# Kernel optimization log

Hardware: AMD Instinct MI355X
Metric: run time of the kernel (lower is better)

The kernel has to match this reference:

```python
import jax, jax.numpy as jnp
import numpy as np


def setup_inputs() -> dict:
    key = jax.random.key(0)
    k1, k2, k3, k4 = jax.random.split(key, 4)
    B, S, D_in, D_out = 4, 4096, 768, 64
    x = jax.random.normal(k1, (B, S, D_in), dtype=jnp.float32)
    # torch nn.Linear stores weight as [out, in]; scale to keep activations sane
    scale = 1.0 / np.sqrt(D_in)
    Wq = jax.random.normal(k2, (D_out, D_in), dtype=jnp.float32) * scale
    Wk = jax.random.normal(k3, (D_out, D_in), dtype=jnp.float32) * scale
    Wv = jax.random.normal(k4, (D_out, D_in), dtype=jnp.float32) * scale
    return {"x": x, "Wq": Wq, "Wk": Wk, "Wv": Wv}


def reference(x, Wq, Wk, Wv):
    # q,k,v: [B,S,D_out] via x @ W.T (torch Linear semantics)
    q = jnp.einsum('bsd,od->bso', x, Wq)
    k = jnp.einsum('bsd,od->bso', x, Wk)
    v = jnp.einsum('bsd,od->bso', x, Wv)
    d_out = k.shape[-1]
    scores = jnp.einsum('bqo,bko->bqk', q, k) / jnp.sqrt(jnp.asarray(d_out, x.dtype))
    weights = jax.nn.softmax(scores, axis=-1)  # [B,S,S]
    return jnp.einsum('bqk,bko->bqo', weights, v)
```

## Files before the change

kernel.cpp:

```cpp
#include <hip/hip_runtime.h>
#include <hip/hip_bf16.h>


typedef __attribute__((ext_vector_type(8))) __bf16 bf16x8;
typedef __attribute__((ext_vector_type(4))) __bf16 bf16x4;
typedef __attribute__((ext_vector_type(4))) float  f32x4;

constexpr int BATCH = 4;
constexpr int SEQ   = 4096;
constexpr int DIN   = 768;
constexpr int NTOT  = 192;
constexpr int MROWS = BATCH * SEQ;
constexpr int KVT   = 64;

__device__ __forceinline__ f32x4 mfma16(bf16x8 a, bf16x8 b, f32x4 c) {
    return __builtin_amdgcn_mfma_f32_16x16x32_bf16(a, b, c, 0, 0, 0);
}

__device__ __forceinline__ void gload_lds16(const void* g, void* l) {
    __builtin_amdgcn_global_load_lds(
        (const __attribute__((address_space(1))) void*)g,
        (__attribute__((address_space(3))) void*)l, 16, 0, 0);
}

__global__ __launch_bounds__(256) void convert_w(
        const float* __restrict__ Wq, const float* __restrict__ Wk,
        const float* __restrict__ Wv, __bf16* __restrict__ wb) {
    int i = blockIdx.x * 256 + threadIdx.x;
    if (i >= NTOT * DIN) return;
    int n = i / DIN;
    const float* src = (n < 64) ? Wq : (n < 128) ? Wk : Wv;
    float scale = (n < 64) ? 0.125f * 1.44269504f : 1.0f;
    wb[i] = (__bf16)(src[(n & 63) * DIN + (i % DIN)] * scale);
}

__global__ __launch_bounds__(512, 2) void qkv_proj(
        const float* __restrict__ x, const __bf16* __restrict__ wb,
        __bf16* __restrict__ q, __bf16* __restrict__ k, __bf16* __restrict__ vT) {
    const int tid  = threadIdx.x;
    const int wave = tid >> 6, lane = tid & 63;
    const int strip = wave & 3, nh = wave >> 2;
    const int lr = lane & 15;
    const int g  = lane >> 4;
    const int rx = (lr & 7) << 4;

    __shared__ __align__(16) char wbuf[3][NTOT * 128];
    __shared__ __align__(16) char xbuf[3][64 * 256];

    const int  srow = lane >> 3;
    const int  ssw  = ((lane & 7) << 4) ^ ((srow & 7) << 4);
    const int  xs4  = lane >> 4;
    const char* wbb = (const char*)wb;
    const char* xbb = (const char*)x;
    const int  xrow0 = blockIdx.x * 64;

    auto stage = [&](int buf, int kt) {
#pragma unroll
        for (int s = 0; s < 3; ++s) {
            const int rbase = wave * 24 + s * 8;
            gload_lds16(wbb + (size_t)(rbase + srow) * (DIN * 2) + kt * 128 + ssw,
                        &wbuf[buf][rbase * 128]);
        }
#pragma unroll
        for (int s = 0; s < 2; ++s) {
            const int xr = wave * 8 + s * 4;
            const int sswx = ((lane & 15) ^ ((xr & 15) + xs4)) << 4;
            gload_lds16(xbb + (size_t)(xrow0 + xr + xs4) * (DIN * 4) +
                            kt * 256 + sswx,
                        &xbuf[buf][xr * 256]);
        }
    };

    f32x4 acc[6];
#pragma unroll
    for (int t = 0; t < 6; ++t) acc[t] = f32x4{0.f, 0.f, 0.f, 0.f};

    stage(0, 0);
    asm volatile("s_waitcnt vmcnt(0) lgkmcnt(0)" ::: "memory");
    __builtin_amdgcn_s_barrier();

    constexpr int NT = DIN / 64;
    int cur = 0, nxt = 1;
    for (int kt = 0; kt < NT; ++kt) {
        stage(nxt, (kt + 1 == NT) ? 0 : kt + 1);
        asm volatile("s_waitcnt vmcnt(5) lgkmcnt(0)" ::: "memory");
        __builtin_amdgcn_s_barrier();

#pragma unroll
        for (int ks = 0; ks < 2; ++ks) {
            const char* xrp = &xbuf[cur][(strip * 16 + lr) * 256];
            f32x4 xa = *(const f32x4*)(xrp + ((ks * 128 + g * 32)      ^ (lr << 4)));
            f32x4 xb = *(const f32x4*)(xrp + ((ks * 128 + g * 32 + 16) ^ (lr << 4)));
            bf16x8 af;
            af[0] = (__bf16)xa[0]; af[1] = (__bf16)xa[1]; af[2] = (__bf16)xa[2]; af[3] = (__bf16)xa[3];
            af[4] = (__bf16)xb[0]; af[5] = (__bf16)xb[1]; af[6] = (__bf16)xb[2]; af[7] = (__bf16)xb[3];
#pragma unroll
            for (int t = 0; t < 6; ++t) {
                const int nr = (nh * 6 + t) * 16 + lr;
                bf16x8 bf = *(const bf16x8*)(&wbuf[cur][nr * 128] +
                                             ((ks * 64 + g * 16) ^ rx));
                acc[t] = mfma16(af, bf, acc[t]);
            }
        }
        cur = nxt; nxt = (nxt == 2) ? 0 : nxt + 1;
    }

    const int orow = blockIdx.x * 64 + strip * 16 + g * 4;
#pragma unroll
    for (int t = 0; t < 6; ++t) {
        int n = (nh * 6 + t) * 16 + lr;
#pragma unroll
        for (int r = 0; r < 4; ++r) {
            int m = orow + r;
            __bf16 hv = (__bf16)acc[t][r];
            if (n < 64) {
                q[(size_t)m * 64 + n] = hv;
            } else if (n < 128) {
                k[(size_t)m * 64 + (n - 64)] = hv;
            } else {
                int b = m >> 12, s = m & (SEQ - 1);
                vT[(size_t)b * 64 * SEQ + (size_t)(n - 128) * SEQ + s] = hv;
            }
        }
    }
}

__global__ __launch_bounds__(512, 2) void attn(
        const __bf16* __restrict__ q, const __bf16* __restrict__ k,
        const __bf16* __restrict__ vT, float* __restrict__ out) {
    const int tid  = threadIdx.x;
    const int wave = tid >> 6, lane = tid & 63;
    const int strip = wave & 3, par = wave >> 2;
    const int b  = blockIdx.y;
    const int q0 = blockIdx.x * 64 + strip * 16;
    const int lr = lane & 15;
    const int g  = lane >> 4;
    const int lk = g * 8;
    const int rx = (lr & 7) << 4;

    const __bf16* qp = q  + (size_t)b * SEQ * 64;
    const __bf16* kp = k  + (size_t)b * SEQ * 64;
    const __bf16* vp = vT + (size_t)b * 64 * SEQ;

    __shared__ __align__(16) char kbuf[3][KVT * 128];
    __shared__ __align__(16) char vbuf[3][KVT * 128];
    __shared__ __align__(16) char pbuf[8][2048];
    char* pw = &pbuf[wave][0];

    const int  srow = lane >> 3;
    const int  ssw  = ((lane & 7) << 4) ^ ((srow & 7) << 4);

    auto stage = [&](int buf, int kv0) {
        gload_lds16((const char*)kp + (size_t)(kv0 + wave * 8 + srow) * 128 + ssw,
                    &kbuf[buf][wave * 8 * 128]);
        gload_lds16((const char*)vp + (size_t)(wave * 8 + srow) * (SEQ * 2) +
                        (size_t)kv0 * 2 + ssw,
                    &vbuf[buf][wave * 8 * 128]);
    };

    bf16x8 qf0 = *(const bf16x8*)(qp + (size_t)(q0 + lr) * 64 + lk);
    bf16x8 qf1 = *(const bf16x8*)(qp + (size_t)(q0 + lr) * 64 + 32 + lk);

    f32x4 acc_o[4];
#pragma unroll
    for (int t = 0; t < 4; ++t) acc_o[t] = f32x4{0.f, 0.f, 0.f, 0.f};
    float l_run = 0.f;

    stage(0, 0);
    asm volatile("s_waitcnt vmcnt(0) lgkmcnt(0)" ::: "memory");
    __builtin_amdgcn_s_barrier();

    constexpr int NT = SEQ / KVT;
    int cur = 0, nxt = 1;
    for (int it = 0; it < NT; ++it) {
        stage(nxt, ((it + 1) & (NT - 1)) * KVT);
        asm volatile("s_waitcnt vmcnt(2) lgkmcnt(0)" ::: "memory");
        __builtin_amdgcn_s_barrier();

        f32x4 s4[2];
#pragma unroll
        for (int j = 0; j < 2; ++j) {
            const char* kr = &kbuf[cur][(par * 32 + j * 16 + lr) * 128];
            bf16x8 kf0 = *(const bf16x8*)(kr + ((g * 16) ^ rx));
            bf16x8 kf1 = *(const bf16x8*)(kr + ((64 + g * 16) ^ rx));
            f32x4 a = f32x4{0.f, 0.f, 0.f, 0.f};
            a = mfma16(kf0, qf0, a);
            a = mfma16(kf1, qf1, a);
            s4[j] = a;
        }

#pragma unroll
        for (int j = 0; j < 2; ++j) {
            bf16x4 pbv;
#pragma unroll
            for (int r = 0; r < 4; ++r) {
                float p = __builtin_amdgcn_exp2f(s4[j][r]);
                l_run += p;
                pbv[r] = (__bf16)p;
            }
            *(bf16x4*)(pw + lr * 128 + ((j * 32 + g * 8) ^ rx)) = pbv;
        }
        asm volatile("s_waitcnt lgkmcnt(0)" ::: "memory");

        bf16x8 pf = *(const bf16x8*)(pw + lr * 128 + ((g * 16) ^ rx));
#pragma unroll
        for (int t = 0; t < 4; ++t) {
            const char* vr = &vbuf[cur][(t * 16 + lr) * 128];
            bf16x8 vf = *(const bf16x8*)(vr + ((par * 64 + g * 16) ^ rx));
            acc_o[t] = mfma16(vf, pf, acc_o[t]);
        }

        cur = nxt; nxt = (nxt == 2) ? 0 : nxt + 1;
    }

    l_run += __shfl_xor(l_run, 16);
    l_run += __shfl_xor(l_run, 32);
    __syncthreads();

    float* mo = (float*)(&pbuf[0][0]) + strip * 1024;
    float* ml = (float*)(&kbuf[0][0]);
    if (par == 1) {
#pragma unroll
        for (int t = 0; t < 4; ++t)
            *(f32x4*)(mo + lr * 64 + t * 16 + g * 4) = acc_o[t];
        if (lane < 16) ml[strip * 16 + lr] = l_run;
    }
    __syncthreads();
    if (par == 0) {
        float inv = 1.f / (l_run + ml[strip * 16 + lr]);
        float* ob = out + ((size_t)b * SEQ + q0 + lr) * 64;
#pragma unroll
        for (int t = 0; t < 4; ++t) {
            f32x4 o1 = *(const f32x4*)(mo + lr * 64 + t * 16 + g * 4);
            f32x4 o4;
#pragma unroll
            for (int r = 0; r < 4; ++r) o4[r] = (acc_o[t][r] + o1[r]) * inv;
            *(f32x4*)(ob + t * 16 + g * 4) = o4;
        }
    }
}

extern "C" void kernel_launch(void* const* d_in, const int* in_sizes, int n_in,
                              void* d_out, int out_size, void* d_ws, size_t ws_size,
                              hipStream_t stream) {
    const float* x  = (const float*)d_in[0];
    const float* Wq = (const float*)d_in[1];
    const float* Wk = (const float*)d_in[2];
    const float* Wv = (const float*)d_in[3];
    float* out = (float*)d_out;

    char* ws = (char*)d_ws;
    __bf16* wb = (__bf16*)(ws);
    __bf16* qb = (__bf16*)(ws + 294912);
    __bf16* kb = (__bf16*)(ws + 294912 + 2097152);
    __bf16* vT = (__bf16*)(ws + 294912 + 2u * 2097152);

    convert_w<<<dim3((NTOT * DIN + 255) / 256), dim3(256), 0, stream>>>(Wq, Wk, Wv, wb);
    qkv_proj<<<dim3(MROWS / 64), dim3(512), 0, stream>>>(x, wb, qb, kb, vT);
    attn<<<dim3(SEQ / 64, BATCH), dim3(512), 0, stream>>>(qb, kb, vT, out);
}
```

Baseline: 62.67 us.

## Split attention KV loop across four wave groups with 128-wide KV tiles

Doubles the attention block to 1024 threads (16 waves) so four parity groups each cover part of a larger 128-row KV tile, and widens the V staging layout to 256-byte rows with a new swizzle. The partial O accumulators and row sums from three groups are reduced through shared memory before normalization. This is meant to add more waves per query strip and cut the number of loop iterations and barriers. In exchange it uses more LDS and a heavier final reduction, and the larger block may lower the number of resident blocks per CU.

```diff
diff --git a/kernel.cpp b/kernel.cpp
--- a/kernel.cpp
+++ b/kernel.cpp
@@ -11,7 +11,7 @@
 constexpr int DIN   = 768;
 constexpr int NTOT  = 192;
 constexpr int MROWS = BATCH * SEQ;
-constexpr int KVT   = 64;
+constexpr int KVT   = 128;
 
 __device__ __forceinline__ f32x4 mfma16(bf16x8 a, bf16x8 b, f32x4 c) {
     return __builtin_amdgcn_mfma_f32_16x16x32_bf16(a, b, c, 0, 0, 0);
@@ -125,7 +125,7 @@
     }
 }
 
-__global__ __launch_bounds__(512, 2) void attn(
+__global__ __launch_bounds__(1024, 4) void attn(
         const __bf16* __restrict__ q, const __bf16* __restrict__ k,
         const __bf16* __restrict__ vT, float* __restrict__ out) {
     const int tid  = threadIdx.x;
@@ -143,19 +143,21 @@
     const __bf16* vp = vT + (size_t)b * 64 * SEQ;
 
     __shared__ __align__(16) char kbuf[3][KVT * 128];
-    __shared__ __align__(16) char vbuf[3][KVT * 128];
-    __shared__ __align__(16) char pbuf[8][2048];
+    __shared__ __align__(16) char vbuf[3][64 * 256];
+    __shared__ __align__(16) char pbuf[16][2048];
     char* pw = &pbuf[wave][0];
 
-    const int  srow = lane >> 3;
-    const int  ssw  = ((lane & 7) << 4) ^ ((srow & 7) << 4);
+    const int  srow8 = lane >> 3;
+    const int  sswK  = ((lane & 7) << 4) ^ ((srow8 & 7) << 4);
+    const int  vrow  = wave * 4 + (lane >> 4);
+    const int  sswV  = ((lane & 15) ^ (vrow & 7)) << 4;
 
     auto stage = [&](int buf, int kv0) {
-        gload_lds16((const char*)kp + (size_t)(kv0 + wave * 8 + srow) * 128 + ssw,
+        gload_lds16((const char*)kp + (size_t)(kv0 + wave * 8 + srow8) * 128 + sswK,
                     &kbuf[buf][wave * 8 * 128]);
-        gload_lds16((const char*)vp + (size_t)(wave * 8 + srow) * (SEQ * 2) +
-                        (size_t)kv0 * 2 + ssw,
-                    &vbuf[buf][wave * 8 * 128]);
+        gload_lds16((const char*)vp + (size_t)vrow * (SEQ * 2) +
+                        (size_t)kv0 * 2 + sswV,
+                    &vbuf[buf][wave * 4 * 256]);
     };
 
     bf16x8 qf0 = *(const bf16x8*)(qp + (size_t)(q0 + lr) * 64 + lk);
@@ -205,7 +207,7 @@
         bf16x8 pf = *(const bf16x8*)(pw + lr * 128 + ((g * 16) ^ rx));
 #pragma unroll
         for (int t = 0; t < 4; ++t) {
-            const char* vr = &vbuf[cur][(t * 16 + lr) * 128];
+            const char* vr = &vbuf[cur][(t * 16 + lr) * 256];
             bf16x8 vf = *(const bf16x8*)(vr + ((par * 64 + g * 16) ^ rx));
             acc_o[t] = mfma16(vf, pf, acc_o[t]);
         }
@@ -217,24 +219,32 @@
     l_run += __shfl_xor(l_run, 32);
     __syncthreads();
 
-    float* mo = (float*)(&pbuf[0][0]) + strip * 1024;
-    float* ml = (float*)(&kbuf[0][0]);
-    if (par == 1) {
+    float* mo = (float*)(&kbuf[0][0]);
+    float* ml = (float*)(&vbuf[0][0]);
+    if (par > 0) {
+        const int pi = par - 1;
+        float* dst = mo + (size_t)((pi * 4 + strip) * 16 + lr) * 64;
 #pragma unroll
         for (int t = 0; t < 4; ++t)
-            *(f32x4*)(mo + lr * 64 + t * 16 + g * 4) = acc_o[t];
-        if (lane < 16) ml[strip * 16 + lr] = l_run;
+            *(f32x4*)(dst + t * 16 + g * 4) = acc_o[t];
+        if (lane < 16) ml[(pi * 4 + strip) * 16 + lr] = l_run;
     }
     __syncthreads();
     if (par == 0) {
-        float inv = 1.f / (l_run + ml[strip * 16 + lr]);
+        float L = l_run;
+#pragma unroll
+        for (int pi = 0; pi < 3; ++pi) L += ml[(pi * 4 + strip) * 16 + lr];
+        float inv = 1.f / L;
         float* ob = out + ((size_t)b * SEQ + q0 + lr) * 64;
 #pragma unroll
         for (int t = 0; t < 4; ++t) {
-            f32x4 o1 = *(const f32x4*)(mo + lr * 64 + t * 16 + g * 4);
-            f32x4 o4;
-#pragma unroll
-            for (int r = 0; r < 4; ++r) o4[r] = (acc_o[t][r] + o1[r]) * inv;
+            f32x4 o4 = acc_o[t];
+#pragma unroll
+            for (int pi = 0; pi < 3; ++pi)
+                o4 += *(const f32x4*)(mo + (size_t)((pi * 4 + strip) * 16 + lr) * 64 +
+                                      t * 16 + g * 4);
+#pragma unroll
+            for (int r = 0; r < 4; ++r) o4[r] *= inv;
             *(f32x4*)(ob + t * 16 + g * 4) = o4;
         }
     }
@@ -257,5 +267,5 @@
 
     convert_w<<<dim3((NTOT * DIN + 255) / 256), dim3(256), 0, stream>>>(Wq, Wk, Wv, wb);
     qkv_proj<<<dim3(MROWS / 64), dim3(512), 0, stream>>>(x, wb, qb, kb, vT);
-    attn<<<dim3(SEQ / 64, BATCH), dim3(512), 0, stream>>>(qb, kb, vT, out);
-}
+    attn<<<dim3(SEQ / 64, BATCH), dim3(1024), 0, stream>>>(qb, kb, vT, out);
+}
```

Measured after the change: 53.77 us. 1.17x faster.
